# Kernel optimization log

Measured on AMD Instinct MI355X. Metric: run time of the kernel, lower is better.

The kernel has to match this reference:

```python
import jax, jax.numpy as jnp
import numpy as np

B, S, HID = 16, 577, 768
H, D = 12, 64          # heads, head_dim
N_KEEP = 576           # kept channels after structured pruning


def setup_inputs() -> dict:
    key = jax.random.key(0)
    ks = jax.random.split(key, 10)
    hs = jax.random.normal(ks[0], (B, S, HID), dtype=jnp.float32)
    Wq = jax.random.normal(ks[1], (HID, N_KEEP), dtype=jnp.float32) * 0.02
    bq = jax.random.normal(ks[2], (N_KEEP,), dtype=jnp.float32) * 0.02
    Wk = jax.random.normal(ks[3], (HID, N_KEEP), dtype=jnp.float32) * 0.02
    bk = jax.random.normal(ks[4], (N_KEEP,), dtype=jnp.float32) * 0.02
    Wv = jax.random.normal(ks[5], (HID, N_KEEP), dtype=jnp.float32) * 0.02
    bv = jax.random.normal(ks[6], (N_KEEP,), dtype=jnp.float32) * 0.02
    # positions of nonzero entries of the boolean padding masks (unique, sorted)
    q_idx = jnp.sort(jax.random.permutation(ks[7], HID)[:N_KEEP]).astype(jnp.int32)
    k_idx = jnp.sort(jax.random.permutation(ks[8], HID)[:N_KEEP]).astype(jnp.int32)
    v_idx = jnp.sort(jax.random.permutation(ks[9], HID)[:N_KEEP]).astype(jnp.int32)
    return {"hidden_states": hs, "Wq": Wq, "bq": bq, "Wk": Wk, "bk": bk,
            "Wv": Wv, "bv": bv, "q_idx": q_idx, "k_idx": k_idx, "v_idx": v_idx}


def _pad_and_split_heads(x, idx):
    # scatter pruned channels [B,S,N_KEEP] back into full layout [B,S,HID],
    # then split into heads -> [B,H,S,D]
    padded = jnp.zeros((B, S, HID), dtype=x.dtype).at[:, :, idx].set(x)
    return padded.reshape(B, S, H, D).transpose(0, 2, 1, 3)


def reference(hidden_states, Wq, bq, Wk, bk, Wv, bv, q_idx, k_idx, v_idx):
    q = hidden_states @ Wq + bq            # [B,S,N_KEEP]
    k = hidden_states @ Wk + bk
    v = hidden_states @ Wv + bv
    ql = _pad_and_split_heads(q, q_idx)     # [B,H,S,D]
    kl = _pad_and_split_heads(k, k_idx)
    vl = _pad_and_split_heads(v, v_idx)
    scale = 1.0 / np.float32(np.sqrt(D))
    scores = jnp.einsum('bhqd,bhkd->bhqk', ql, kl) * scale  # [B,H,S,S]
    probs = jax.nn.softmax(scores, axis=-1)
    ctx = jnp.einsum('bhqk,bhkd->bhqd', probs, vl)          # [B,H,S,D]
    ctx = ctx.transpose(0, 2, 1, 3).reshape(B, S, HID)       # [B,S,HID]
    return ctx[:, :, v_idx]                                  # gather kept channels
```

## Files before the change

### kernel.cpp

```cpp
#include <hip/hip_runtime.h>
#include <hip/hip_bf16.h>
#include <cstdint>
#include <cstddef>

#define B_     16
#define S_     577
#define HID_   768
#define H_     12
#define D_     64
#define NKEEP_ 576
#define MROWS  (B_ * S_)
#define BHROWS (B_ * H_ * S_)

typedef __bf16 bf16;
typedef __bf16 bf16x8 __attribute__((ext_vector_type(8)));
typedef float  f32x4  __attribute__((ext_vector_type(4)));

__device__ __forceinline__ void gload16(const bf16* g, bf16* l) {
    __builtin_amdgcn_global_load_lds(
        (const __attribute__((address_space(1))) unsigned int*)g,
        (__attribute__((address_space(3))) unsigned int*)l, 16, 0, 0);
}

__device__ __forceinline__ float fexp2(float x) {
#if __has_builtin(__builtin_amdgcn_exp2f)
    return __builtin_amdgcn_exp2f(x);
#else
    return exp2f(x);
#endif
}

#define WAITBAR(N) asm volatile("s_waitcnt vmcnt(" #N ") lgkmcnt(0)\n\ts_barrier" ::: "memory")

#define FMAX2 17.3123405f

__global__ __launch_bounds__(256) void k_cvt(const float* __restrict__ src,
                                             bf16* __restrict__ dst, int n4) {
    int i = blockIdx.x * 256 + threadIdx.x;
    if (i >= n4) return;
    float4 v = reinterpret_cast<const float4*>(src)[i];
    union { bf16 h[4]; uint2 u; } o;
    o.h[0] = (bf16)v.x; o.h[1] = (bf16)v.y; o.h[2] = (bf16)v.z; o.h[3] = (bf16)v.w;
    reinterpret_cast<uint2*>(dst)[i] = o.u;
}

__global__ void k_inv(const int* __restrict__ qi, const int* __restrict__ ki,
                      const int* __restrict__ vi,
                      const float* __restrict__ bq, const float* __restrict__ bk,
                      const float* __restrict__ bv,
                      int* __restrict__ inv, float* __restrict__ bias_p) {
    int p = blockIdx.x, t = threadIdx.x;
    inv[p * HID_ + t] = -1;
    bias_p[p * HID_ + t] = 0.0f;
    __syncthreads();
    const int* src = (p == 0) ? qi : (p == 1) ? ki : vi;
    const float* bb = (p == 0) ? bq : (p == 1) ? bk : bv;
    if (t < NKEEP_) {
        inv[p * HID_ + src[t]] = t;
        bias_p[p * HID_ + src[t]] = bb[t];
    }
}

__global__ __launch_bounds__(256) void k_wt(const float* __restrict__ Wq,
                                            const float* __restrict__ Wk,
                                            const float* __restrict__ Wv,
                                            const int* __restrict__ qi,
                                            const int* __restrict__ ki,
                                            const int* __restrict__ vi,
                                            bf16* __restrict__ Wp_t) {
    __shared__ float tile[64][33];
    const int p = blockIdx.y;
    const int j0 = blockIdx.x * 32;
    const float* W  = (p == 0) ? Wq : (p == 1) ? Wk : Wv;
    const int* idx  = (p == 0) ? qi : (p == 1) ? ki : vi;
    bf16* dst = Wp_t + (size_t)p * HID_ * HID_;
    const int t = threadIdx.x;
    const int lj = t & 31, lk = t >> 5;
    const int sj = t >> 3, ke = (t & 7) * 8;
    const int c = idx[j0 + sj];
    for (int kt = 0; kt < HID_; kt += 64) {
        __syncthreads();
#pragma unroll
        for (int i = 0; i < 8; ++i)
            tile[lk + i * 8][lj] = W[(size_t)(kt + lk + i * 8) * NKEEP_ + j0 + lj];
        __syncthreads();
        union { bf16 h[8]; bf16x8 v; } o;
#pragma unroll
        for (int i = 0; i < 8; ++i) o.h[i] = (bf16)tile[ke + i][sj];
        *reinterpret_cast<bf16x8*>(dst + (size_t)c * HID_ + kt + ke) = o.v;
    }
}

#define BM 128
#define BN 256
#define BK 32
#define NT 24
#define BUFE 12288

__global__ __launch_bounds__(256, 2) void k_gemm(const bf16* __restrict__ X,
                                                 const bf16* __restrict__ Wp_t,
                                                 const float* __restrict__ bias_p,
                                                 bf16* __restrict__ Qo, bf16* __restrict__ Ko,
                                                 bf16* __restrict__ Vo) {
    __shared__ bf16 smem[3 * BUFE];

    const int xcd = blockIdx.x & 7, pos = blockIdx.x >> 3;
    const int L = xcd * 82 + (xcd > 0 ? 1 : 0) + pos;
    const int m0 = (L / 9) * BM;
    const int np = L % 9;
    const int n0 = (np % 3) * BN;
    const int p  = np / 3;

    const bf16* Wbase = Wp_t + (size_t)p * HID_ * HID_;
    bf16* Obase = (p == 0) ? Qo : (p == 1) ? Ko : Vo;
    const float osc = (p == 0) ? 0.125f * 1.44269504f : 1.0f;

    const int t = threadIdx.x;
    const int wid = t >> 6, lane = t & 63;
    const int wr = wid >> 1, wc = wid & 1;
    const int lrow = lane & 15, g = lane >> 4, lk = (lane >> 4) * 8;
    const int srow = lane >> 2, scol = (lane & 3) * 8;

    const bf16* Xs = X + (size_t)m0 * HID_;
    const bf16* Ws = Wbase + (size_t)n0 * HID_;

    f32x4 acc[4][8] = {};

#define STAGE(buf, kk)                                                          \
    {                                                                           \
        _Pragma("unroll")                                                       \
        for (int i_ = 0; i_ < 2; ++i_) {                                        \
            const int c_ = wid * 2 + i_;                                        \
            gload16(Xs + (size_t)(c_ * 16 + srow) * HID_ + (kk) + scol,         \
                    smem + (buf) * BUFE + c_ * 512);                            \
        }                                                                       \
        _Pragma("unroll")                                                       \
        for (int i_ = 0; i_ < 4; ++i_) {                                        \
            const int c_ = wid * 4 + i_;                                        \
            gload16(Ws + (size_t)(c_ * 16 + srow) * HID_ + (kk) + scol,         \
                    smem + (buf) * BUFE + 4096 + c_ * 512);                     \
        }                                                                       \
    }

#define COMPUTE(buf)                                                            \
    {                                                                           \
        const bf16* As_ = smem + (buf) * BUFE;                                  \
        const bf16* Bs_ = As_ + 4096;                                           \
        bf16x8 af[4], bfr[8];                                                   \
        _Pragma("unroll")                                                       \
        for (int m = 0; m < 4; ++m)                                             \
            af[m] = *reinterpret_cast<const bf16x8*>(                           \
                &As_[(wr * 64 + m * 16 + lrow) * BK + lk]);                     \
        _Pragma("unroll")                                                       \
        for (int n = 0; n < 8; ++n)                                             \
            bfr[n] = *reinterpret_cast<const bf16x8*>(                          \
                &Bs_[(wc * 128 + n * 16 + lrow) * BK + lk]);                    \
        _Pragma("unroll")                                                       \
        for (int m = 0; m < 4; ++m)                                             \
            _Pragma("unroll")                                                   \
            for (int n = 0; n < 8; ++n)                                         \
                acc[m][n] = __builtin_amdgcn_mfma_f32_16x16x32_bf16(            \
                    af[m], bfr[n], acc[m][n], 0, 0, 0);                         \
    }

    STAGE(0, 0)
    STAGE(1, BK)
    WAITBAR(6);

    int kk_next = 2 * BK;
    for (int u = 0; u < 7; ++u) {
#pragma unroll
        for (int j = 0; j < 3; ++j) {
            STAGE((j + 2) % 3, kk_next)
            COMPUTE(j)
            WAITBAR(6);
            kk_next += BK;
        }
    }
    STAGE(2, 23 * BK)
    COMPUTE(0)
    WAITBAR(6);
    COMPUTE(1)
    WAITBAR(0);
    COMPUTE(2)
#undef STAGE
#undef COMPUTE

    float bias_n[8];
#pragma unroll
    for (int n = 0; n < 8; ++n)
        bias_n[n] = bias_p[p * HID_ + n0 + wc * 128 + n * 16 + lrow];

    const int rowl = t >> 2, cq = t & 3;
#pragma unroll
    for (int half = 0; half < 2; ++half) {
        __syncthreads();
        if (wr == half) {
#pragma unroll
            for (int n = 0; n < 8; ++n)
#pragma unroll
                for (int m = 0; m < 4; ++m)
#pragma unroll
                    for (int r = 0; r < 4; ++r)
                        smem[(m * 16 + g * 4 + r) * 260 + wc * 128 + n * 16 + lrow] =
                            (bf16)((acc[m][n][r] + bias_n[n]) * osc);
        }
        __syncthreads();
        const int grow = m0 + half * 64 + rowl;
        if (grow < MROWS) {
            const int b = grow / S_, s = grow % S_;
            const size_t rbase = ((size_t)b * H_ * S_ + s) * D_;
#pragma unroll
            for (int i = 0; i < 8; ++i) {
                const int c0 = i * 32 + cq * 8;
                bf16x8 v = *reinterpret_cast<const bf16x8*>(&smem[rowl * 260 + c0]);
                const int c = n0 + c0, h = c >> 6, d = c & 63;
                *reinterpret_cast<bf16x8*>(&Obase[rbase + (size_t)h * S_ * D_ + d]) = v;
            }
        }
    }
}

#define KB2  64
#define VLD2 72
#define KVSZ (KB2 * VLD2)

__global__ __launch_bounds__(512, 4) void k_attn(const bf16* __restrict__ Q,
                                                 const bf16* __restrict__ K,
                                                 const bf16* __restrict__ V,
                                                 const int* __restrict__ inv,
                                                 float* __restrict__ out) {
    __shared__ bf16 Ksm[2][KVSZ];
    __shared__ bf16 Vsm[2][KVSZ];

    const int bid = blockIdx.x;
    const int bh = bid % (B_ * H_);
    const int q0 = (bid / (B_ * H_)) * 128;
    const int t = threadIdx.x, wid = t >> 6, lane = t & 63;
    const int lcol = lane & 15, g = lane >> 4;

    const bf16* Qb = Q + (size_t)bh * S_ * D_;
    const bf16* Kb = K + (size_t)bh * S_ * D_;
    const bf16* Vb = V + (size_t)bh * S_ * D_;

    const int qrow = q0 + wid * 16 + lcol;
    bf16x8 qf0 = {}, qf1 = {};
    if (qrow < S_) {
        qf0 = *reinterpret_cast<const bf16x8*>(Qb + (size_t)qrow * D_ + g * 8);
        qf1 = *reinterpret_cast<const bf16x8*>(Qb + (size_t)qrow * D_ + 32 + g * 8);
    }

    const int key_t = t >> 3;
    const int a_t = t & 7;
    const int ch_t = a_t * 8;
    const int ks_s = key_t >> 4, g_s = (key_t >> 2) & 3, r_s = key_t & 3;
    const int pos = (ks_s >> 1) * 32 + g_s * 8 + (ks_s & 1) * 4 + r_s;

    float lrun = 0.f;
    f32x4 oT[4] = {};
    const bf16x8 zv = {};

    bf16x8 kreg = zv, vreg = zv;
    if (key_t < S_) {
        kreg = *reinterpret_cast<const bf16x8*>(Kb + (size_t)key_t * D_ + ch_t);
        vreg = *reinterpret_cast<const bf16x8*>(Vb + (size_t)key_t * D_ + ch_t);
    }

    int cur = 0;
    for (int k0 = 0; k0 < S_; k0 += KB2) {
        *reinterpret_cast<bf16x8*>(&Ksm[cur][key_t * VLD2 + ch_t]) = kreg;
#pragma unroll
        for (int i = 0; i < 8; ++i) {
            int ch = (pos >> 3) ^ i ^ a_t;
            Vsm[cur][(ch_t + i) * VLD2 + ch * 8 + (pos & 7)] = vreg[i];
        }
        __syncthreads();

        if (k0 + KB2 < S_) {
            int gk = k0 + KB2 + key_t;
            if (gk < S_) {
                kreg = *reinterpret_cast<const bf16x8*>(Kb + (size_t)gk * D_ + ch_t);
                vreg = *reinterpret_cast<const bf16x8*>(Vb + (size_t)gk * D_ + ch_t);
            } else { kreg = zv; vreg = zv; }
        }

        f32x4 sv[4];
        __builtin_amdgcn_s_setprio(1);
#pragma unroll
        for (int ks = 0; ks < 4; ++ks) {
            const bf16* kr = &Ksm[cur][(ks * 16 + lcol) * VLD2];
            bf16x8 kf0 = *reinterpret_cast<const bf16x8*>(kr + g * 8);
            bf16x8 kf1 = *reinterpret_cast<const bf16x8*>(kr + 32 + g * 8);
            f32x4 z = {-FMAX2, -FMAX2, -FMAX2, -FMAX2};
            z = __builtin_amdgcn_mfma_f32_16x16x32_bf16(kf0, qf0, z, 0, 0, 0);
            z = __builtin_amdgcn_mfma_f32_16x16x32_bf16(kf1, qf1, z, 0, 0, 0);
            sv[ks] = z;
        }
        __builtin_amdgcn_s_setprio(0);
        if (k0 + KB2 > S_) {
#pragma unroll
            for (int ks = 0; ks < 4; ++ks)
#pragma unroll
                for (int r = 0; r < 4; ++r)
                    if (k0 + ks * 16 + g * 4 + r >= S_) sv[ks][r] = -INFINITY;
        }

        union { bf16 h[16]; bf16x8 v[2]; } pu;
        float rs = 0.f;
#pragma unroll
        for (int ks = 0; ks < 4; ++ks)
#pragma unroll
            for (int r = 0; r < 4; ++r) {
                float pv = fexp2(sv[ks][r]);
                rs += pv;
                pu.h[ks * 4 + r] = (bf16)pv;
            }
        lrun += rs;

        __builtin_amdgcn_s_setprio(1);
#pragma unroll
        for (int kh = 0; kh < 2; ++kh) {
#pragma unroll
            for (int tt = 0; tt < 4; ++tt) {
                int d = tt * 16 + lcol;
                int s3 = (d ^ (d >> 3)) & 7;
                int ch = (kh * 4 + g) ^ s3;
                bf16x8 vf = *reinterpret_cast<const bf16x8*>(&Vsm[cur][d * VLD2 + ch * 8]);
                oT[tt] = __builtin_amdgcn_mfma_f32_16x16x32_bf16(vf, pu.v[kh], oT[tt], 0, 0, 0);
            }
        }
        __builtin_amdgcn_s_setprio(0);
        cur ^= 1;
    }

    lrun += __shfl_xor(lrun, 16);
    lrun += __shfl_xor(lrun, 32);

    if (qrow < S_) {
        const int b = bh / H_, h = bh % H_;
        const int* invv = inv + 2 * HID_;
        float invl = 1.0f / lrun;
        float* orow = out + ((size_t)b * S_ + qrow) * NKEEP_;
#pragma unroll
        for (int tt = 0; tt < 4; ++tt)
#pragma unroll
            for (int r = 0; r < 4; ++r) {
                int d = tt * 16 + g * 4 + r;
                int j = invv[h * D_ + d];
                if (j >= 0) orow[j] = oT[tt][r] * invl;
            }
    }
}

extern "C" void kernel_launch(void* const* d_in, const int* in_sizes, int n_in,
                              void* d_out, int out_size, void* d_ws, size_t ws_size,
                              hipStream_t stream) {
    const float* hs = (const float*)d_in[0];
    const float* Wq = (const float*)d_in[1];
    const float* bq = (const float*)d_in[2];
    const float* Wk = (const float*)d_in[3];
    const float* bk = (const float*)d_in[4];
    const float* Wv = (const float*)d_in[5];
    const float* bv = (const float*)d_in[6];
    const int* qi = (const int*)d_in[7];
    const int* ki = (const int*)d_in[8];
    const int* vi = (const int*)d_in[9];
    float* out = (float*)d_out;

    char* ws = (char*)d_ws;
    size_t off = 0;
    bf16* hs_bf = (bf16*)(ws + off); off += (size_t)MROWS * HID_ * 2;
    bf16* Wp_t  = (bf16*)(ws + off); off += (size_t)3 * HID_ * HID_ * 2;
    float* bias_p = (float*)(ws + off); off += 3 * HID_ * 4;
    int* inv = (int*)(ws + off); off += 3 * HID_ * 4;
    bf16* Qw = (bf16*)(ws + off); off += (size_t)BHROWS * D_ * 2;
    bf16* Kw = (bf16*)(ws + off); off += (size_t)BHROWS * D_ * 2;
    bf16* Vw = (bf16*)(ws + off); off += (size_t)BHROWS * D_ * 2;

    const int n4 = MROWS * HID_ / 4;
    hipMemsetAsync(Wp_t, 0, (size_t)3 * HID_ * HID_ * 2, stream);
    k_cvt<<<(n4 + 255) / 256, 256, 0, stream>>>(hs, hs_bf, n4);
    k_inv<<<3, HID_, 0, stream>>>(qi, ki, vi, bq, bk, bv, inv, bias_p);
    k_wt<<<dim3(NKEEP_ / 32, 3), 256, 0, stream>>>(Wq, Wk, Wv, qi, ki, vi, Wp_t);
    k_gemm<<<657, 256, 0, stream>>>(hs_bf, Wp_t, bias_p, Qw, Kw, Vw);
    k_attn<<<5 * B_ * H_, 512, 0, stream>>>(Qw, Kw, Vw, inv, out);
}
```

Before: 114.1 us.

## Process two query tiles per wave in attention, halving block size

The attention kernel now runs 4 waves per block instead of 8. Each wave handles 32 query rows as two 16-row MFMA tiles, so every K and V fragment read from LDS feeds twice as many MFMAs. The K/V staging is spread over fewer threads, each loading 16 channels, and the constant score offset previously used to seed the QK accumulator is dropped. This cuts LDS read traffic per FLOP. In exchange it doubles accumulator and probability registers per lane, leaves fewer resident waves to hide latency, and removes the exp2 range guard.

```diff
diff --git a/kernel.cpp b/kernel.cpp
--- a/kernel.cpp
+++ b/kernel.cpp
@@ -31,8 +31,6 @@
 }
 
 #define WAITBAR(N) asm volatile("s_waitcnt vmcnt(" #N ") lgkmcnt(0)\n\ts_barrier" ::: "memory")
-
-#define FMAX2 17.3123405f
 
 __global__ __launch_bounds__(256) void k_cvt(const float* __restrict__ src,
                                              bf16* __restrict__ dst, int n4) {
@@ -225,7 +223,7 @@
 #define VLD2 72
 #define KVSZ (KB2 * VLD2)
 
-__global__ __launch_bounds__(512, 4) void k_attn(const bf16* __restrict__ Q,
+__global__ __launch_bounds__(256, 4) void k_attn(const bf16* __restrict__ Q,
                                                  const bf16* __restrict__ K,
                                                  const bf16* __restrict__ V,
                                                  const int* __restrict__ inv,
@@ -243,58 +241,77 @@
     const bf16* Kb = K + (size_t)bh * S_ * D_;
     const bf16* Vb = V + (size_t)bh * S_ * D_;
 
-    const int qrow = q0 + wid * 16 + lcol;
-    bf16x8 qf0 = {}, qf1 = {};
-    if (qrow < S_) {
-        qf0 = *reinterpret_cast<const bf16x8*>(Qb + (size_t)qrow * D_ + g * 8);
-        qf1 = *reinterpret_cast<const bf16x8*>(Qb + (size_t)qrow * D_ + 32 + g * 8);
-    }
-
-    const int key_t = t >> 3;
-    const int a_t = t & 7;
-    const int ch_t = a_t * 8;
+    const int qrowA = q0 + wid * 32 + lcol;
+    const int qrowB = qrowA + 16;
+    bf16x8 qf0a = {}, qf1a = {}, qf0b = {}, qf1b = {};
+    if (qrowA < S_) {
+        qf0a = *reinterpret_cast<const bf16x8*>(Qb + (size_t)qrowA * D_ + g * 8);
+        qf1a = *reinterpret_cast<const bf16x8*>(Qb + (size_t)qrowA * D_ + 32 + g * 8);
+    }
+    if (qrowB < S_) {
+        qf0b = *reinterpret_cast<const bf16x8*>(Qb + (size_t)qrowB * D_ + g * 8);
+        qf1b = *reinterpret_cast<const bf16x8*>(Qb + (size_t)qrowB * D_ + 32 + g * 8);
+    }
+
+    const int key_t = t >> 2;
+    const int ch16 = (t & 3) * 16;
     const int ks_s = key_t >> 4, g_s = (key_t >> 2) & 3, r_s = key_t & 3;
     const int pos = (ks_s >> 1) * 32 + g_s * 8 + (ks_s & 1) * 4 + r_s;
-
-    float lrun = 0.f;
-    f32x4 oT[4] = {};
+    const int ph = pos >> 3, pl = pos & 7;
+
+    float lrunA = 0.f, lrunB = 0.f;
+    f32x4 oTA[4] = {}, oTB[4] = {};
     const bf16x8 zv = {};
 
-    bf16x8 kreg = zv, vreg = zv;
-    if (key_t < S_) {
-        kreg = *reinterpret_cast<const bf16x8*>(Kb + (size_t)key_t * D_ + ch_t);
-        vreg = *reinterpret_cast<const bf16x8*>(Vb + (size_t)key_t * D_ + ch_t);
-    }
+    bf16x8 kr0, kr1, vr0, vr1;
+    kr0 = *reinterpret_cast<const bf16x8*>(Kb + (size_t)key_t * D_ + ch16);
+    kr1 = *reinterpret_cast<const bf16x8*>(Kb + (size_t)key_t * D_ + ch16 + 8);
+    vr0 = *reinterpret_cast<const bf16x8*>(Vb + (size_t)key_t * D_ + ch16);
+    vr1 = *reinterpret_cast<const bf16x8*>(Vb + (size_t)key_t * D_ + ch16 + 8);
 
     int cur = 0;
     for (int k0 = 0; k0 < S_; k0 += KB2) {
-        *reinterpret_cast<bf16x8*>(&Ksm[cur][key_t * VLD2 + ch_t]) = kreg;
+        *reinterpret_cast<bf16x8*>(&Ksm[cur][key_t * VLD2 + ch16]) = kr0;
+        *reinterpret_cast<bf16x8*>(&Ksm[cur][key_t * VLD2 + ch16 + 8]) = kr1;
 #pragma unroll
         for (int i = 0; i < 8; ++i) {
-            int ch = (pos >> 3) ^ i ^ a_t;
-            Vsm[cur][(ch_t + i) * VLD2 + ch * 8 + (pos & 7)] = vreg[i];
+            int d = ch16 + i;
+            int ch = ph ^ (d & 7) ^ (d >> 3);
+            Vsm[cur][d * VLD2 + ch * 8 + pl] = vr0[i];
+        }
+#pragma unroll
+        for (int i = 0; i < 8; ++i) {
+            int d = ch16 + 8 + i;
+            int ch = ph ^ (d & 7) ^ (d >> 3);
+            Vsm[cur][d * VLD2 + ch * 8 + pl] = vr1[i];
         }
         __syncthreads();
 
         if (k0 + KB2 < S_) {
             int gk = k0 + KB2 + key_t;
             if (gk < S_) {
-                kreg = *reinterpret_cast<const bf16x8*>(Kb + (size_t)gk * D_ + ch_t);
-                vreg = *reinterpret_cast<const bf16x8*>(Vb + (size_t)gk * D_ + ch_t);
-            } else { kreg = zv; vreg = zv; }
-        }
-
-        f32x4 sv[4];
+                kr0 = *reinterpret_cast<const bf16x8*>(Kb + (size_t)gk * D_ + ch16);
+                kr1 = *reinterpret_cast<const bf16x8*>(Kb + (size_t)gk * D_ + ch16 + 8);
+                vr0 = *reinterpret_cast<const bf16x8*>(Vb + (size_t)gk * D_ + ch16);
+                vr1 = *reinterpret_cast<const bf16x8*>(Vb + (size_t)gk * D_ + ch16 + 8);
+            } else { kr0 = zv; kr1 = zv; vr0 = zv; vr1 = zv; }
+        }
+
+        f32x4 svA[4], svB[4];
         __builtin_amdgcn_s_setprio(1);
 #pragma unroll
         for (int ks = 0; ks < 4; ++ks) {
             const bf16* kr = &Ksm[cur][(ks * 16 + lcol) * VLD2];
             bf16x8 kf0 = *reinterpret_cast<const bf16x8*>(kr + g * 8);
             bf16x8 kf1 = *reinterpret_cast<const bf16x8*>(kr + 32 + g * 8);
-            f32x4 z = {-FMAX2, -FMAX2, -FMAX2, -FMAX2};
-            z = __builtin_amdgcn_mfma_f32_16x16x32_bf16(kf0, qf0, z, 0, 0, 0);
-            z = __builtin_amdgcn_mfma_f32_16x16x32_bf16(kf1, qf1, z, 0, 0, 0);
-            sv[ks] = z;
+            f32x4 za = {};
+            za = __builtin_amdgcn_mfma_f32_16x16x32_bf16(kf0, qf0a, za, 0, 0, 0);
+            za = __builtin_amdgcn_mfma_f32_16x16x32_bf16(kf1, qf1a, za, 0, 0, 0);
+            svA[ks] = za;
+            f32x4 zb = {};
+            zb = __builtin_amdgcn_mfma_f32_16x16x32_bf16(kf0, qf0b, zb, 0, 0, 0);
+            zb = __builtin_amdgcn_mfma_f32_16x16x32_bf16(kf1, qf1b, zb, 0, 0, 0);
+            svB[ks] = zb;
         }
         __builtin_amdgcn_s_setprio(0);
         if (k0 + KB2 > S_) {
@@ -302,20 +319,25 @@
             for (int ks = 0; ks < 4; ++ks)
 #pragma unroll
                 for (int r = 0; r < 4; ++r)
-                    if (k0 + ks * 16 + g * 4 + r >= S_) sv[ks][r] = -INFINITY;
-        }
-
-        union { bf16 h[16]; bf16x8 v[2]; } pu;
-        float rs = 0.f;
+                    if (k0 + ks * 16 + g * 4 + r >= S_) {
+                        svA[ks][r] = -INFINITY;
+                        svB[ks][r] = -INFINITY;
+                    }
+        }
+
+        union { bf16 h[16]; bf16x8 v[2]; } puA, puB;
+        float rsA = 0.f, rsB = 0.f;
 #pragma unroll
         for (int ks = 0; ks < 4; ++ks)
 #pragma unroll
             for (int r = 0; r < 4; ++r) {
-                float pv = fexp2(sv[ks][r]);
-                rs += pv;
-                pu.h[ks * 4 + r] = (bf16)pv;
+                float pa = fexp2(svA[ks][r]);
+                float pb = fexp2(svB[ks][r]);
+                rsA += pa; rsB += pb;
+                puA.h[ks * 4 + r] = (bf16)pa;
+                puB.h[ks * 4 + r] = (bf16)pb;
             }
-        lrun += rs;
+        lrunA += rsA; lrunB += rsB;
 
         __builtin_amdgcn_s_setprio(1);
 #pragma unroll
@@ -326,28 +348,43 @@
                 int s3 = (d ^ (d >> 3)) & 7;
                 int ch = (kh * 4 + g) ^ s3;
                 bf16x8 vf = *reinterpret_cast<const bf16x8*>(&Vsm[cur][d * VLD2 + ch * 8]);
-                oT[tt] = __builtin_amdgcn_mfma_f32_16x16x32_bf16(vf, pu.v[kh], oT[tt], 0, 0, 0);
+                oTA[tt] = __builtin_amdgcn_mfma_f32_16x16x32_bf16(vf, puA.v[kh], oTA[tt], 0, 0, 0);
+                oTB[tt] = __builtin_amdgcn_mfma_f32_16x16x32_bf16(vf, puB.v[kh], oTB[tt], 0, 0, 0);
             }
         }
         __builtin_amdgcn_s_setprio(0);
         cur ^= 1;
     }
 
-    lrun += __shfl_xor(lrun, 16);
-    lrun += __shfl_xor(lrun, 32);
-
-    if (qrow < S_) {
-        const int b = bh / H_, h = bh % H_;
-        const int* invv = inv + 2 * HID_;
-        float invl = 1.0f / lrun;
-        float* orow = out + ((size_t)b * S_ + qrow) * NKEEP_;
+    lrunA += __shfl_xor(lrunA, 16);
+    lrunA += __shfl_xor(lrunA, 32);
+    lrunB += __shfl_xor(lrunB, 16);
+    lrunB += __shfl_xor(lrunB, 32);
+
+    const int b = bh / H_, h = bh % H_;
+    const int* invv = inv + 2 * HID_;
+    if (qrowA < S_) {
+        float invl = 1.0f / lrunA;
+        float* orow = out + ((size_t)b * S_ + qrowA) * NKEEP_;
 #pragma unroll
         for (int tt = 0; tt < 4; ++tt)
 #pragma unroll
             for (int r = 0; r < 4; ++r) {
                 int d = tt * 16 + g * 4 + r;
                 int j = invv[h * D_ + d];
-                if (j >= 0) orow[j] = oT[tt][r] * invl;
+                if (j >= 0) orow[j] = oTA[tt][r] * invl;
+            }
+    }
+    if (qrowB < S_) {
+        float invl = 1.0f / lrunB;
+        float* orow = out + ((size_t)b * S_ + qrowB) * NKEEP_;
+#pragma unroll
+        for (int tt = 0; tt < 4; ++tt)
+#pragma unroll
+            for (int r = 0; r < 4; ++r) {
+                int d = tt * 16 + g * 4 + r;
+                int j = invv[h * D_ + d];
+                if (j >= 0) orow[j] = oTB[tt][r] * invl;
             }
     }
 }
@@ -383,5 +420,5 @@
     k_inv<<<3, HID_, 0, stream>>>(qi, ki, vi, bq, bk, bv, inv, bias_p);
     k_wt<<<dim3(NKEEP_ / 32, 3), 256, 0, stream>>>(Wq, Wk, Wv, qi, ki, vi, Wp_t);
     k_gemm<<<657, 256, 0, stream>>>(hs_bf, Wp_t, bias_p, Qw, Kw, Vw);
-    k_attn<<<5 * B_ * H_, 512, 0, stream>>>(Qw, Kw, Vw, inv, out);
-}
+    k_attn<<<5 * B_ * H_, 256, 0, stream>>>(Qw, Kw, Vw, inv, out);
+}
```

After: 141.3 us. 1.24x slower.
